# Optimization experiments

Hardware: AMD Instinct MI355X
Metric: run time of the kernel (lower is better)

The kernel has to match this reference:

```python
import jax, jax.numpy as jnp
import numpy as np

B, L, D = 2, 2048, 2048
H, G, E = 16, 4, 128       # num_heads, group_num, head dim
KV = H // G                # kv heads = 4
OUT = D                    # output_dim == input_dim for residual


def setup_inputs() -> dict:
    key = jax.random.key(0)
    ks = jax.random.split(key, 12)
    s_in = 1.0 / np.sqrt(D)
    s_o = 1.0 / np.sqrt(H * E)
    return {
        "x": jax.random.normal(ks[0], (B, L, D), jnp.float32),
        "Wq": jax.random.normal(ks[1], (D, H * E), jnp.float32) * s_in,
        "bq": jnp.zeros((H * E,), jnp.float32),
        "Wk": jax.random.normal(ks[2], (D, KV * E), jnp.float32) * s_in,
        "bk": jnp.zeros((KV * E,), jnp.float32),
        "Wv": jax.random.normal(ks[3], (D, KV * E), jnp.float32) * s_in,
        "bv": jnp.zeros((KV * E,), jnp.float32),
        "Wo": jax.random.normal(ks[4], (H * E, OUT), jnp.float32) * s_o,
        "bo": jnp.zeros((OUT,), jnp.float32),
        "gamma": jnp.ones((OUT,), jnp.float32),
        "beta": jnp.zeros((OUT,), jnp.float32),
    }


def reference(x, Wq, bq, Wk, bk, Wv, bv, Wo, bo, gamma, beta):
    b, l, _ = x.shape
    Q = (x @ Wq + bq).reshape(b, l, H, E)            # [B,L,H,E]
    K = (x @ Wk + bk).reshape(b, l, KV, E)           # [B,L,KV,E]
    V = (x @ Wv + bv).reshape(b, l, KV, E)
    # GQA expand: reshape(B,L,1,KV,E).expand(G) -> head h = g*KV + kv (tile kv heads G times)
    K = jnp.broadcast_to(K[:, :, None, :, :], (b, l, G, KV, E)).reshape(b, l, H, E)
    V = jnp.broadcast_to(V[:, :, None, :, :], (b, l, G, KV, E)).reshape(b, l, H, E)
    scores = jnp.einsum('blhe,bmhe->bhlm', Q, K) / np.sqrt(E).astype(np.float32)
    # causal mask: triu(ones, diag=1) * -1e9 added to scores
    mask = jnp.triu(jnp.ones((l, l), jnp.float32), k=1) * (-1e9)
    attn = jax.nn.softmax(scores + mask[None, None, :, :], axis=-1)
    ctx = jnp.einsum('bhlm,bmhe->blhe', attn, V).reshape(b, l, H * E)
    y = jax.nn.gelu(ctx @ Wo + bo, approximate=False)  # nn.GELU default = exact erf
    r = x + y
    mu = jnp.mean(r, axis=-1, keepdims=True)
    var = jnp.var(r, axis=-1, keepdims=True)
    return (r - mu) * jax.lax.rsqrt(var + 1e-5) * gamma + beta
```

## Files before the change

### kernel.cpp

```cpp
#include <hip/hip_runtime.h>
#include <hip/hip_bf16.h>
#include <math.h>

typedef __bf16 bf16_t;
typedef __bf16 bf16x4 __attribute__((ext_vector_type(4)));
typedef __bf16 bf16x8 __attribute__((ext_vector_type(8)));
typedef float  f32x4  __attribute__((ext_vector_type(4)));
typedef float  f32x16 __attribute__((ext_vector_type(16)));

#define MFMA16(a,b,c) __builtin_amdgcn_mfma_f32_16x16x32_bf16((a),(b),(c),0,0,0)
#define MFMA32(a,b,c) __builtin_amdgcn_mfma_f32_32x32x16_bf16((a),(b),(c),0,0,0)

#define B_ 2
#define L_ 2048
#define D_ 2048
#define H_ 16
#define KV_ 4
#define E_ 128
#define M_ (B_*L_)
#define NQKV_ 3072

__device__ __forceinline__ void async_ld16(const bf16_t* g, bf16_t* l) {
    __builtin_amdgcn_global_load_lds((const __attribute__((address_space(1))) void*)g,
                                     (__attribute__((address_space(3))) void*)l, 16, 0, 0);
}

__global__ __launch_bounds__(256) void cast_bias_kernel(const float* __restrict__ src,
                                                        bf16_t* __restrict__ dst,
                                                        const float* __restrict__ bq,
                                                        const float* __restrict__ bk,
                                                        const float* __restrict__ bv,
                                                        float* __restrict__ qbias) {
    int bid = blockIdx.x;
    if (bid < 8192) {
        int i = (bid * 256 + threadIdx.x) * 4;
        float4 v = *(const float4*)(src + i);
        bf16x4 o;
        o.x = (bf16_t)v.x; o.y = (bf16_t)v.y; o.z = (bf16_t)v.z; o.w = (bf16_t)v.w;
        *(bf16x4*)(dst + i) = o;
    } else {
        int i = (bid - 8192) * 256 + threadIdx.x;
        if (i < 2048) qbias[i] = bq[i];
        else if (i < 2560) qbias[i] = bk[i - 2048];
        else if (i < 3072) qbias[i] = bv[i - 2560];
    }
}

__global__ __launch_bounds__(256) void wtrans_kernel(const float* __restrict__ Wq,
                                                     const float* __restrict__ Wk,
                                                     const float* __restrict__ Wv,
                                                     const float* __restrict__ Wo,
                                                     bf16_t* __restrict__ WqkvT,
                                                     bf16_t* __restrict__ WoT) {
    __shared__ float tile[32][33];
    int bx = blockIdx.x;
    const float* W; bf16_t* WT; int N, n0;
    if (bx < 64)      { W = Wq; WT = WqkvT;                  N = 2048; n0 = bx * 32; }
    else if (bx < 80) { W = Wk; WT = WqkvT + 2048 * 2048;    N = 512;  n0 = (bx - 64) * 32; }
    else if (bx < 96) { W = Wv; WT = WqkvT + 2560 * 2048;    N = 512;  n0 = (bx - 80) * 32; }
    else              { W = Wo; WT = WoT;                    N = 2048; n0 = (bx - 96) * 32; }
    int k0 = blockIdx.y * 32;
    int tx = threadIdx.x, ty = threadIdx.y;
    #pragma unroll
    for (int i = 0; i < 32; i += 8)
        tile[ty + i][tx] = W[(size_t)(k0 + ty + i) * N + n0 + tx];
    __syncthreads();
    #pragma unroll
    for (int i = 0; i < 32; i += 8)
        WT[(size_t)(n0 + ty + i) * 2048 + k0 + tx] = (bf16_t)tile[tx][ty + i];
}

template <bool GELU, bool VSPLIT>
__global__ __launch_bounds__(256) void gemm_kernel(const bf16_t* __restrict__ A,
                                                   const bf16_t* __restrict__ BT,
                                                   const float* __restrict__ bias,
                                                   bf16_t* __restrict__ C,
                                                   bf16_t* __restrict__ Vt,
                                                   int M, int N, int K) {
    __shared__ __align__(16) bf16_t sA[128][64];
    __shared__ __align__(16) bf16_t sB[128][64];
    int tid = threadIdx.x;
    int wave = tid >> 6, lane = tid & 63;
    int l16 = lane & 15, quad = lane >> 4;
    int flat = blockIdx.y * gridDim.x + blockIdx.x;
    int cpx = (gridDim.x * gridDim.y) >> 3;
    int swz = (flat & 7) * cpx + (flat >> 3);
    int col0 = (swz % gridDim.x) * 128;
    int row0 = (swz / gridDim.x) * 128;
    int wm = (wave >> 1) * 64;
    int wn = (wave & 1) * 64;

    f32x4 acc[4][4];
    #pragma unroll
    for (int i = 0; i < 4; ++i)
        #pragma unroll
        for (int j = 0; j < 4; ++j)
            acc[i][j] = f32x4{0.f, 0.f, 0.f, 0.f};

    for (int k0 = 0; k0 < K; k0 += 64) {
        #pragma unroll
        for (int c = 0; c < 4; ++c) {
            int ch = c * 256 + tid;
            int r = ch >> 3, cp = ch & 7;
            int cl = cp ^ (r & 7);
            async_ld16(&A[(size_t)(row0 + r) * K + k0 + cl * 8], &sA[r][cp * 8]);
            async_ld16(&BT[(size_t)(col0 + r) * K + k0 + cl * 8], &sB[r][cp * 8]);
        }
        __syncthreads();
        #pragma unroll
        for (int kk = 0; kk < 2; ++kk) {
            bf16x8 af[4], bf[4];
            #pragma unroll
            for (int mt = 0; mt < 4; ++mt) {
                int r = wm + mt * 16 + l16;
                af[mt] = *(const bf16x8*)&sA[r][((kk * 4 + quad) ^ (r & 7)) * 8];
            }
            #pragma unroll
            for (int nt = 0; nt < 4; ++nt) {
                int r = wn + nt * 16 + l16;
                bf[nt] = *(const bf16x8*)&sB[r][((kk * 4 + quad) ^ (r & 7)) * 8];
            }
            #pragma unroll
            for (int mt = 0; mt < 4; ++mt)
                #pragma unroll
                for (int nt = 0; nt < 4; ++nt)
                    acc[mt][nt] = MFMA16(af[mt], bf[nt], acc[mt][nt]);
        }
        __syncthreads();
    }

    #pragma unroll
    for (int mt = 0; mt < 4; ++mt) {
        #pragma unroll
        for (int nt = 0; nt < 4; ++nt) {
            int gcol = col0 + wn + nt * 16 + l16;
            float bv = bias[gcol];
            float vv[4];
            #pragma unroll
            for (int r = 0; r < 4; ++r) {
                float v = acc[mt][nt][r] + bv;
                if (GELU) v = 0.5f * v * (1.f + erff(v * 0.70710678118654752f));
                vv[r] = v;
            }
            int grow0 = row0 + wm + mt * 16 + quad * 4;
            if (VSPLIT && gcol >= 2560) {
                int b = grow0 >> 11, l = grow0 & 2047;
                bf16x4 ov;
                #pragma unroll
                for (int r = 0; r < 4; ++r) ov[r] = (bf16_t)vv[r];
                *(bf16x4*)&Vt[((size_t)(b * 512) + (gcol - 2560)) * L_ + l] = ov;
            } else {
                #pragma unroll
                for (int r = 0; r < 4; ++r)
                    C[(size_t)(grow0 + r) * N + gcol] = (bf16_t)vv[r];
            }
        }
    }
}

__global__ __launch_bounds__(128, 2) void attn_kernel(const bf16_t* __restrict__ QKV,
                                                      const bf16_t* __restrict__ Vt,
                                                      bf16_t* __restrict__ Ctx) {
    __shared__ __align__(16) bf16_t sK[2][64][128];

    const int tid = threadIdx.x;
    const int wave = tid >> 6, lane = tid & 63;
    const int l31 = lane & 31, half = lane >> 5;

    const int idx = blockIdx.x;
    const int rr = idx >> 5;
    const int bh = idx & 31;
    const int u = (rr < 8) ? 31 - rr : (rr < 16) ? rr - 8 : (rr < 24) ? 39 - rr : rr - 16;
    const int h = bh & 15, b = bh >> 4;
    const int kv = h & 3;

    const bf16_t* Kbase = QKV + (size_t)b * L_ * NQKV_ + 2048 + kv * 128;
    const bf16_t* Vbase = Vt + (size_t)(b * 4 + kv) * 128 * L_;
    const float SC = 0.12754995f;

    const int qrow = u * 64 + wave * 32 + l31;

    bf16x8 qf[8];
    const bf16_t* Qrow = QKV + (size_t)(b * L_ + qrow) * NQKV_ + h * 128 + half * 8;
    #pragma unroll
    for (int et = 0; et < 8; ++et) qf[et] = *(const bf16x8*)&Qrow[et * 16];

    f32x16 acc[4];
    #pragma unroll
    for (int em = 0; em < 4; ++em)
        #pragma unroll
        for (int j = 0; j < 16; ++j) acc[em][j] = 0.f;
    float l_i = 0.f;

    #define STAGE_K(KT, BUF)                                                          \
        {                                                                             \
            int kk = (KT) * 64;                                                       \
            _Pragma("unroll")                                                         \
            for (int rep = 0; rep < 8; ++rep) {                                       \
                int ch = rep * 128 + tid;                                             \
                int rk = ch >> 4;                                                     \
                int sc = (ch & 15) ^ (rk & 15);                                       \
                async_ld16(&Kbase[(size_t)(kk + rk) * NQKV_ + sc * 8],                \
                           ((bf16_t*)sK[BUF]) + (size_t)ch * 8);                      \
            }                                                                         \
        }

    STAGE_K(0, 0);
    __syncthreads();

    for (int kt = 0; kt <= u; ++kt) {
        const int bufi = kt & 1;
        if (kt < u) STAGE_K(kt + 1, bufi ^ 1);

        bf16x8 vr[16];
        #pragma unroll
        for (int kc = 0; kc < 4; ++kc)
            #pragma unroll
            for (int em = 0; em < 4; ++em)
                vr[kc * 4 + em] = *(const bf16x8*)&Vbase[(size_t)(em * 32 + l31) * L_ +
                                                         kt * 64 + (kc * 2 + half) * 8];

        f32x16 s[2];
        #pragma unroll
        for (int mt = 0; mt < 2; ++mt)
            #pragma unroll
            for (int j = 0; j < 16; ++j) s[mt][j] = 0.f;
        __builtin_amdgcn_s_setprio(1);
        #pragma unroll
        for (int mt = 0; mt < 2; ++mt)
            #pragma unroll
            for (int et = 0; et < 8; ++et) {
                bf16x8 kf = *(const bf16x8*)&sK[bufi][mt * 32 + l31][((et * 2 + half) ^ (l31 & 15)) * 8];
                s[mt] = MFMA32(kf, qf[et], s[mt]);
            }
        __builtin_amdgcn_s_setprio(0);

        if (kt == u) {
            #pragma unroll
            for (int mt = 0; mt < 2; ++mt)
                #pragma unroll
                for (int j = 0; j < 16; ++j) {
                    int kidx = kt * 64 + mt * 32 + (j & 3) + 8 * (j >> 2) + 4 * half;
                    if (kidx > qrow) s[mt][j] = -3.0e38f;
                }
        }

        float rs = 0.f;
        #pragma unroll
        for (int mt = 0; mt < 2; ++mt)
            #pragma unroll
            for (int j = 0; j < 16; ++j) {
                float p = exp2f(s[mt][j] * SC);
                s[mt][j] = p;
                rs += p;
            }
        rs += __shfl_xor(rs, 32, 64);
        l_i += rs;

        bf16x4 pk[2][4];
        #pragma unroll
        for (int mt = 0; mt < 2; ++mt)
            #pragma unroll
            for (int g = 0; g < 4; ++g) {
                bf16x4 tt;
                #pragma unroll
                for (int i = 0; i < 4; ++i) tt[i] = (bf16_t)s[mt][g * 4 + i];
                pk[mt][g] = tt;
            }

        #pragma unroll
        for (int kc = 0; kc < 4; ++kc) {
            const int mts = kc >> 1, g0 = 2 * (kc & 1);
            bf16x4 send = half ? pk[mts][g0] : pk[mts][g0 + 1];
            bf16x4 keep = half ? pk[mts][g0 + 1] : pk[mts][g0];
            union { bf16x4 v; int i[2]; } su, ru;
            su.v = send;
            ru.i[0] = __shfl_xor(su.i[0], 32, 64);
            ru.i[1] = __shfl_xor(su.i[1], 32, 64);
            bf16x4 lo = half ? ru.v : keep;
            bf16x4 hi = half ? keep : ru.v;
            bf16x8 pf = __builtin_shufflevector(lo, hi, 0, 1, 2, 3, 4, 5, 6, 7);
            __builtin_amdgcn_s_setprio(1);
            #pragma unroll
            for (int em = 0; em < 4; ++em)
                acc[em] = MFMA32(vr[kc * 4 + em], pf, acc[em]);
            __builtin_amdgcn_s_setprio(0);
        }

        __syncthreads();
    }

    const float inv = 1.f / l_i;
    bf16_t* Cp = Ctx + (size_t)(b * L_ + qrow) * 2048 + h * 128;
    #pragma unroll
    for (int em = 0; em < 4; ++em)
        #pragma unroll
        for (int g = 0; g < 4; ++g) {
            bf16x4 ov;
            #pragma unroll
            for (int i = 0; i < 4; ++i) ov[i] = (bf16_t)(acc[em][g * 4 + i] * inv);
            *(bf16x4*)&Cp[em * 32 + g * 8 + half * 4] = ov;
        }
}

__global__ __launch_bounds__(256) void ln_kernel(const bf16_t* __restrict__ Y,
                                                 const float* __restrict__ X,
                                                 const float* __restrict__ gamma,
                                                 const float* __restrict__ beta,
                                                 float* __restrict__ out) {
    __shared__ float sr[2048];
    __shared__ float wred[8];
    size_t row = blockIdx.x;
    const bf16_t* y = Y + row * 2048;
    const float* x = X + row * 2048;
    float sum = 0.f, ssq = 0.f;
    #pragma unroll
    for (int c = 0; c < 2; ++c) {
        int i = (c * 256 + threadIdx.x) * 4;
        bf16x4 yv = *(const bf16x4*)(y + i);
        float4 xv = *(const float4*)(x + i);
        float r0 = xv.x + (float)yv[0];
        float r1 = xv.y + (float)yv[1];
        float r2 = xv.z + (float)yv[2];
        float r3 = xv.w + (float)yv[3];
        sr[i] = r0; sr[i + 1] = r1; sr[i + 2] = r2; sr[i + 3] = r3;
        sum += r0 + r1 + r2 + r3;
        ssq += r0 * r0 + r1 * r1 + r2 * r2 + r3 * r3;
    }
    #pragma unroll
    for (int off = 32; off > 0; off >>= 1) {
        sum += __shfl_xor(sum, off, 64);
        ssq += __shfl_xor(ssq, off, 64);
    }
    int wv = threadIdx.x >> 6;
    if ((threadIdx.x & 63) == 0) { wred[wv] = sum; wred[wv + 4] = ssq; }
    __syncthreads();
    sum = wred[0] + wred[1] + wred[2] + wred[3];
    ssq = wred[4] + wred[5] + wred[6] + wred[7];
    float mu = sum * (1.f / 2048.f);
    float var = ssq * (1.f / 2048.f) - mu * mu;
    float rstd = rsqrtf(var + 1e-5f);
    #pragma unroll
    for (int c = 0; c < 2; ++c) {
        int i = (c * 256 + threadIdx.x) * 4;
        float4 gv = *(const float4*)(gamma + i);
        float4 bv = *(const float4*)(beta + i);
        float4 o;
        o.x = (sr[i]     - mu) * rstd * gv.x + bv.x;
        o.y = (sr[i + 1] - mu) * rstd * gv.y + bv.y;
        o.z = (sr[i + 2] - mu) * rstd * gv.z + bv.z;
        o.w = (sr[i + 3] - mu) * rstd * gv.w + bv.w;
        *(float4*)(out + row * 2048 + i) = o;
    }
}

extern "C" void kernel_launch(void* const* d_in, const int* in_sizes, int n_in,
                              void* d_out, int out_size, void* d_ws, size_t ws_size,
                              hipStream_t stream) {
    const float* x     = (const float*)d_in[0];
    const float* Wq    = (const float*)d_in[1];
    const float* bq    = (const float*)d_in[2];
    const float* Wk    = (const float*)d_in[3];
    const float* bk    = (const float*)d_in[4];
    const float* Wv    = (const float*)d_in[5];
    const float* bv    = (const float*)d_in[6];
    const float* Wo    = (const float*)d_in[7];
    const float* bo    = (const float*)d_in[8];
    const float* gamma = (const float*)d_in[9];
    const float* beta  = (const float*)d_in[10];
    float* out = (float*)d_out;

    char* ws = (char*)d_ws;
    size_t off = 0;
    bf16_t* xb    = (bf16_t*)(ws + off); off += 16777216;
    bf16_t* WqkvT = (bf16_t*)(ws + off); off += 12582912;
    bf16_t* WoT   = (bf16_t*)(ws + off); off += 8388608;
    float*  qbias = (float*)(ws + off);  off += 12288;
    bf16_t* QKV   = (bf16_t*)(ws + off); off += 25165824;
    bf16_t* Vt    = (bf16_t*)(ws + off); off += 4194304;
    bf16_t* Cb    = (bf16_t*)(ws + off); off += 16777216;
    bf16_t* Yb    = (bf16_t*)(ws + off); off += 16777216;

    cast_bias_kernel<<<8204, 256, 0, stream>>>(x, xb, bq, bk, bv, qbias);
    wtrans_kernel<<<dim3(160, 64), dim3(32, 8), 0, stream>>>(Wq, Wk, Wv, Wo, WqkvT, WoT);

    gemm_kernel<false, true><<<dim3(24, 32), 256, 0, stream>>>(xb, WqkvT, qbias, QKV, Vt, M_, NQKV_, D_);
    attn_kernel<<<1024, 128, 0, stream>>>(QKV, Vt, Cb);
    gemm_kernel<true, false><<<dim3(16, 32), 256, 0, stream>>>(Cb, WoT, bo, Yb, nullptr, M_, D_, 2048);
    ln_kernel<<<M_, 256, 0, stream>>>(Yb, x, gamma, beta, out);
}
```

Baseline: 339.0 us.

## Merge prep kernels and use permlane32 swap for P fragment exchange

Folds the input cast, bias copy and weight transpose/cast into one prep kernel launch, removing a launch and its gap. In attention, the two cross-half shuffles per P fragment are replaced with v_permlane32_swap_b32 inline asm. The per-tile row-sum shuffle is deferred to a single reduction after the loop. This relies on the swap yielding the same lo/hi arrangement as the old shuffle code, and on gfx950 supporting the instruction.

```diff
diff --git a/kernel.cpp b/kernel.cpp
--- a/kernel.cpp
+++ b/kernel.cpp
@@ -25,12 +25,19 @@
                                      (__attribute__((address_space(3))) void*)l, 16, 0, 0);
 }
 
-__global__ __launch_bounds__(256) void cast_bias_kernel(const float* __restrict__ src,
-                                                        bf16_t* __restrict__ dst,
-                                                        const float* __restrict__ bq,
-                                                        const float* __restrict__ bk,
-                                                        const float* __restrict__ bv,
-                                                        float* __restrict__ qbias) {
+__global__ __launch_bounds__(256) void prep_kernel(const float* __restrict__ src,
+                                                   bf16_t* __restrict__ dst,
+                                                   const float* __restrict__ bq,
+                                                   const float* __restrict__ bk,
+                                                   const float* __restrict__ bv,
+                                                   float* __restrict__ qbias,
+                                                   const float* __restrict__ Wq,
+                                                   const float* __restrict__ Wk,
+                                                   const float* __restrict__ Wv,
+                                                   const float* __restrict__ Wo,
+                                                   bf16_t* __restrict__ WqkvT,
+                                                   bf16_t* __restrict__ WoT) {
+    __shared__ float tile[32][33];
     int bid = blockIdx.x;
     if (bid < 8192) {
         int i = (bid * 256 + threadIdx.x) * 4;
@@ -38,36 +45,29 @@
         bf16x4 o;
         o.x = (bf16_t)v.x; o.y = (bf16_t)v.y; o.z = (bf16_t)v.z; o.w = (bf16_t)v.w;
         *(bf16x4*)(dst + i) = o;
-    } else {
+    } else if (bid < 8204) {
         int i = (bid - 8192) * 256 + threadIdx.x;
         if (i < 2048) qbias[i] = bq[i];
         else if (i < 2560) qbias[i] = bk[i - 2048];
         else if (i < 3072) qbias[i] = bv[i - 2560];
-    }
-}
-
-__global__ __launch_bounds__(256) void wtrans_kernel(const float* __restrict__ Wq,
-                                                     const float* __restrict__ Wk,
-                                                     const float* __restrict__ Wv,
-                                                     const float* __restrict__ Wo,
-                                                     bf16_t* __restrict__ WqkvT,
-                                                     bf16_t* __restrict__ WoT) {
-    __shared__ float tile[32][33];
-    int bx = blockIdx.x;
-    const float* W; bf16_t* WT; int N, n0;
-    if (bx < 64)      { W = Wq; WT = WqkvT;                  N = 2048; n0 = bx * 32; }
-    else if (bx < 80) { W = Wk; WT = WqkvT + 2048 * 2048;    N = 512;  n0 = (bx - 64) * 32; }
-    else if (bx < 96) { W = Wv; WT = WqkvT + 2560 * 2048;    N = 512;  n0 = (bx - 80) * 32; }
-    else              { W = Wo; WT = WoT;                    N = 2048; n0 = (bx - 96) * 32; }
-    int k0 = blockIdx.y * 32;
-    int tx = threadIdx.x, ty = threadIdx.y;
-    #pragma unroll
-    for (int i = 0; i < 32; i += 8)
-        tile[ty + i][tx] = W[(size_t)(k0 + ty + i) * N + n0 + tx];
-    __syncthreads();
-    #pragma unroll
-    for (int i = 0; i < 32; i += 8)
-        WT[(size_t)(n0 + ty + i) * 2048 + k0 + tx] = (bf16_t)tile[tx][ty + i];
+    } else {
+        int g = bid - 8204;
+        int bx = g % 160;
+        int k0 = (g / 160) * 32;
+        const float* W; bf16_t* WT; int N, n0;
+        if (bx < 64)      { W = Wq; WT = WqkvT;                  N = 2048; n0 = bx * 32; }
+        else if (bx < 80) { W = Wk; WT = WqkvT + 2048 * 2048;    N = 512;  n0 = (bx - 64) * 32; }
+        else if (bx < 96) { W = Wv; WT = WqkvT + 2560 * 2048;    N = 512;  n0 = (bx - 80) * 32; }
+        else              { W = Wo; WT = WoT;                    N = 2048; n0 = (bx - 96) * 32; }
+        int tx = threadIdx.x & 31, ty = threadIdx.x >> 5;
+        #pragma unroll
+        for (int i = 0; i < 32; i += 8)
+            tile[ty + i][tx] = W[(size_t)(k0 + ty + i) * N + n0 + tx];
+        __syncthreads();
+        #pragma unroll
+        for (int i = 0; i < 32; i += 8)
+            WT[(size_t)(n0 + ty + i) * 2048 + k0 + tx] = (bf16_t)tile[tx][ty + i];
+    }
 }
 
 template <bool GELU, bool VSPLIT>
@@ -254,7 +254,6 @@
                 s[mt][j] = p;
                 rs += p;
             }
-        rs += __shfl_xor(rs, 32, 64);
         l_i += rs;
 
         bf16x4 pk[2][4];
@@ -271,15 +270,12 @@
         #pragma unroll
         for (int kc = 0; kc < 4; ++kc) {
             const int mts = kc >> 1, g0 = 2 * (kc & 1);
-            bf16x4 send = half ? pk[mts][g0] : pk[mts][g0 + 1];
-            bf16x4 keep = half ? pk[mts][g0 + 1] : pk[mts][g0];
-            union { bf16x4 v; int i[2]; } su, ru;
-            su.v = send;
-            ru.i[0] = __shfl_xor(su.i[0], 32, 64);
-            ru.i[1] = __shfl_xor(su.i[1], 32, 64);
-            bf16x4 lo = half ? ru.v : keep;
-            bf16x4 hi = half ? keep : ru.v;
-            bf16x8 pf = __builtin_shufflevector(lo, hi, 0, 1, 2, 3, 4, 5, 6, 7);
+            union { bf16x4 v; int i[2]; } a, bb;
+            a.v = pk[mts][g0];
+            bb.v = pk[mts][g0 + 1];
+            asm("v_permlane32_swap_b32 %0, %1" : "+v"(a.i[0]), "+v"(bb.i[0]));
+            asm("v_permlane32_swap_b32 %0, %1" : "+v"(a.i[1]), "+v"(bb.i[1]));
+            bf16x8 pf = __builtin_shufflevector(a.v, bb.v, 0, 1, 2, 3, 4, 5, 6, 7);
             __builtin_amdgcn_s_setprio(1);
             #pragma unroll
             for (int em = 0; em < 4; ++em)
@@ -290,6 +286,7 @@
         __syncthreads();
     }
 
+    l_i += __shfl_xor(l_i, 32, 64);
     const float inv = 1.f / l_i;
     bf16_t* Cp = Ctx + (size_t)(b * L_ + qrow) * 2048 + h * 128;
     #pragma unroll
@@ -381,8 +378,8 @@
     bf16_t* Cb    = (bf16_t*)(ws + off); off += 16777216;
     bf16_t* Yb    = (bf16_t*)(ws + off); off += 16777216;
 
-    cast_bias_kernel<<<8204, 256, 0, stream>>>(x, xb, bq, bk, bv, qbias);
-    wtrans_kernel<<<dim3(160, 64), dim3(32, 8), 0, stream>>>(Wq, Wk, Wv, Wo, WqkvT, WoT);
+    prep_kernel<<<18444, 256, 0, stream>>>(x, xb, bq, bk, bv, qbias,
+                                           Wq, Wk, Wv, Wo, WqkvT, WoT);
 
     gemm_kernel<false, true><<<dim3(24, 32), 256, 0, stream>>>(xb, WqkvT, qbias, QKV, Vt, M_, NQKV_, D_);
     attn_kernel<<<1024, 128, 0, stream>>>(QKV, Vt, Cb);
```

Result: no change. 332.8 us, median of 3 (-1.8%).
